# Kernel tuning notes

Hardware: AMD Instinct MI355X
Metric: run time of the kernel (lower is better)

The kernel has to match this reference:

```python
import jax, jax.numpy as jnp
import numpy as np

B, N, D = 2, 2048, 768
H = 12
HD = D // H  # 64

def setup_inputs() -> dict:
    key = jax.random.key(0)
    ks = jax.random.split(key, 5)
    scale = 1.0 / np.sqrt(D)
    return {
        "x": jax.random.normal(ks[0], (B, N, D), dtype=jnp.float32),
        "W_kqv": jax.random.normal(ks[1], (H, 3 * HD, D), dtype=jnp.float32) * scale,
        "b_kqv": jax.random.normal(ks[2], (H, 3 * HD), dtype=jnp.float32) * 0.01,
        "W_proj": jax.random.normal(ks[3], (D, D), dtype=jnp.float32) * scale,
        "b_proj": jax.random.normal(ks[4], (D,), dtype=jnp.float32) * 0.01,
    }

def reference(x, W_kqv, b_kqv, W_proj, b_proj):
    # Per-head Linear: x @ W_h^T + b_h, all heads at once -> [B, H, N, 3*HD]
    kqv = jnp.einsum('bnd,hod->bhno', x, W_kqv) + b_kqv[None, :, None, :]
    k, q, v = jnp.split(kqv, 3, axis=-1)  # each [B, H, N, HD]
    # scores = q @ k^T / sqrt(head_dim)  (attention_scores(a=k, b=q))
    scores = jnp.einsum('bhqd,bhkd->bhqk', q, k) / jnp.sqrt(jnp.asarray(HD, x.dtype))
    # causal mask (tril): masked_fill with -inf where mask == 0
    causal = jnp.tril(jnp.ones((N, N), dtype=bool))
    scores = jnp.where(causal[None, None, :, :], scores, -jnp.inf)
    attn = jax.nn.softmax(scores, axis=-1)
    sa = jnp.einsum('bhqk,bhkd->bhqd', attn, v)  # [B, H, N, HD]
    # concat heads along feature dim (head order preserved)
    sa = sa.transpose(0, 2, 1, 3).reshape(B, N, D)
    # output projection
    return sa @ W_proj.T + b_proj
```

## Files before the change

kernel.cpp:

```cpp
#include <hip/hip_runtime.h>

#define BB 2
#define SEQ 2048
#define DIM 768
#define NH 12
#define HD 64

typedef _Float16 half8 __attribute__((ext_vector_type(8)));
typedef _Float16 h4v __attribute__((ext_vector_type(4)));
typedef __fp16 f16x2 __attribute__((ext_vector_type(2)));
typedef float floatx4 __attribute__((ext_vector_type(4)));

__device__ __forceinline__ void gl_lds16(const _Float16* g, _Float16* l) {
    __builtin_amdgcn_global_load_lds(
        (const __attribute__((address_space(1))) void*)g,
        (__attribute__((address_space(3))) void*)l, 16, 0, 0);
}

__device__ __forceinline__ h4v pack4(float a, float b, float c, float d) {
    union { f16x2 h2[2]; h4v h4; } u;
    u.h2[0] = __builtin_amdgcn_cvt_pkrtz(a, b);
    u.h2[1] = __builtin_amdgcn_cvt_pkrtz(c, d);
    return u.h4;
}

__global__ __launch_bounds__(256)
void cvt3(const float* __restrict__ s0, _Float16* __restrict__ d0, int nb0,
          const float* __restrict__ s1, _Float16* __restrict__ d1, int nb1,
          const float* __restrict__ s2, _Float16* __restrict__ d2) {
    int b = blockIdx.x;
    const float* s; _Float16* d;
    if (b < nb0)            { s = s0; d = d0; }
    else if (b < nb0 + nb1) { s = s1; d = d1; b -= nb0; }
    else                    { s = s2; d = d2; b -= nb0 + nb1; }
    const int i = (b * 256 + threadIdx.x) * 8;
    float4 a = *(const float4*)(s + i);
    float4 c = *(const float4*)(s + i + 4);
    half8 h;
    h[0] = (_Float16)a.x; h[1] = (_Float16)a.y; h[2] = (_Float16)a.z; h[3] = (_Float16)a.w;
    h[4] = (_Float16)c.x; h[5] = (_Float16)c.y; h[6] = (_Float16)c.z; h[7] = (_Float16)c.w;
    *(half8*)(d + i) = h;
}

#define GEMM_CORE_P(APTR, BPTR)                                                 \
    __shared__ _Float16 Asl[3][128 * 32];                                       \
    __shared__ _Float16 Bsl[3][128 * 32];                                       \
    const int t = threadIdx.x, w = t >> 6, lane = t & 63;                       \
    const int quad = lane >> 4, l15 = lane & 15;                                \
    const int wm = w >> 1, wn = w & 1;                                          \
    const floatx4 z4 = {0.f, 0.f, 0.f, 0.f};                                    \
    floatx4 acc[4][4];                                                          \
    _Pragma("unroll") for (int i = 0; i < 4; ++i)                               \
        _Pragma("unroll") for (int j = 0; j < 4; ++j) acc[i][j] = z4;           \
    const _Float16* pA = APTR + (size_t)(m0 + w * 32 + l15) * DIM + quad * 8;   \
    const _Float16* pB = BPTR + (size_t)(c0 + w * 32 + l15) * DIM + quad * 8;   \
    _Pragma("unroll") for (int pt = 0; pt < 2; ++pt) {                          \
        gl_lds16(pA + pt * 32,            &Asl[pt][(w * 2 + 0) * 512]);         \
        gl_lds16(pA + pt * 32 + 16 * DIM, &Asl[pt][(w * 2 + 1) * 512]);         \
        gl_lds16(pB + pt * 32,            &Bsl[pt][(w * 2 + 0) * 512]);         \
        gl_lds16(pB + pt * 32 + 16 * DIM, &Bsl[pt][(w * 2 + 1) * 512]);         \
    }                                                                           \
    int cur = 0, pre = 2;                                                       \
    for (int it = 0; it < DIM / 32; ++it) {                                     \
        if (it + 1 < DIM / 32)                                                  \
            asm volatile("s_waitcnt vmcnt(4) lgkmcnt(0)" ::: "memory");         \
        else                                                                    \
            asm volatile("s_waitcnt vmcnt(0) lgkmcnt(0)" ::: "memory");         \
        __builtin_amdgcn_s_barrier();                                           \
        __builtin_amdgcn_sched_barrier(0);                                      \
        if (it + 2 < DIM / 32) {                                                \
            const int k2 = (it + 2) * 32;                                       \
            gl_lds16(pA + k2,            &Asl[pre][(w * 2 + 0) * 512]);         \
            gl_lds16(pA + k2 + 16 * DIM, &Asl[pre][(w * 2 + 1) * 512]);         \
            gl_lds16(pB + k2,            &Bsl[pre][(w * 2 + 0) * 512]);         \
            gl_lds16(pB + k2 + 16 * DIM, &Bsl[pre][(w * 2 + 1) * 512]);         \
        }                                                                       \
        half8 af[4], bf[4];                                                     \
        _Pragma("unroll") for (int i = 0; i < 4; ++i)                           \
            af[i] = *(const half8*)&Asl[cur][(wm * 4 + i) * 512 + lane * 8];    \
        _Pragma("unroll") for (int j = 0; j < 4; ++j)                           \
            bf[j] = *(const half8*)&Bsl[cur][(wn * 4 + j) * 512 + lane * 8];    \
        _Pragma("unroll") for (int i = 0; i < 4; ++i)                           \
            _Pragma("unroll") for (int j = 0; j < 4; ++j)                       \
                acc[i][j] = __builtin_amdgcn_mfma_f32_16x16x32_f16(             \
                    af[i], bf[j], acc[i][j], 0, 0, 0);                          \
        cur = (cur == 2) ? 0 : cur + 1;                                         \
        pre = (pre == 2) ? 0 : pre + 1;                                         \
    }

__global__ __launch_bounds__(256)
void kqv_gemm2(const _Float16* __restrict__ xh, const _Float16* __restrict__ Wh,
               const float* __restrict__ bias, _Float16* __restrict__ kb,
               _Float16* __restrict__ qb, _Float16* __restrict__ vbT) {
    const int hw = blockIdx.x;
    const int lg = (hw & 7) * 72 + (hw >> 3);
    const int m0 = (lg / 18) * 128, c0 = (lg % 18) * 128;
    GEMM_CORE_P(xh, Wh)
    #pragma unroll
    for (int j = 0; j < 4; ++j) {
        const int cbase = c0 + (wn * 4 + j) * 16;
        const int h = cbase / 192;
        const int rem = cbase - h * 192;
        const int part = rem >> 6;
        const float bv = bias[cbase + l15];
        const int d = (rem & 63) + l15;
        if (part == 2) {
            const int bidx = m0 >> 11;
            const int nb = (m0 & (SEQ - 1)) + wm * 64 + quad * 4;
            _Float16* vdst = vbT + ((size_t)(bidx * NH + h) * HD + d) * SEQ;
            #pragma unroll
            for (int i = 0; i < 4; ++i)
                *(h4v*)&vdst[nb + i * 16] =
                    pack4(acc[i][j][0] + bv, acc[i][j][1] + bv,
                          acc[i][j][2] + bv, acc[i][j][3] + bv);
        } else {
            _Float16* dst = (part == 0) ? kb : qb;
            #pragma unroll
            for (int i = 0; i < 4; ++i)
                #pragma unroll
                for (int r = 0; r < 4; ++r) {
                    const int m = m0 + (wm * 4 + i) * 16 + quad * 4 + r;
                    const int bidx = m >> 11, n = m & (SEQ - 1);
                    dst[(((size_t)(bidx * NH + h) * SEQ + n) << 6) + d] =
                        (_Float16)(acc[i][j][r] + bv);
                }
        }
    }
}

__global__ __launch_bounds__(256)
void proj_gemm2(const _Float16* __restrict__ A, const _Float16* __restrict__ Wh,
                const float* __restrict__ bias, float* __restrict__ out) {
    const int hw = blockIdx.x;
    const int lg = (hw & 7) * 24 + (hw >> 3);
    const int m0 = (lg / 6) * 128, c0 = (lg % 6) * 128;
    GEMM_CORE_P(A, Wh)
    #pragma unroll
    for (int j = 0; j < 4; ++j) {
        const int cbase = c0 + (wn * 4 + j) * 16;
        const float bv = bias[cbase + l15];
        #pragma unroll
        for (int i = 0; i < 4; ++i)
            #pragma unroll
            for (int r = 0; r < 4; ++r) {
                const int m = m0 + (wm * 4 + i) * 16 + quad * 4 + r;
                out[(size_t)m * DIM + cbase + l15] = acc[i][j][r] + bv;
            }
    }
}

__global__ __launch_bounds__(256)
void attn_mfma(const _Float16* __restrict__ qb, const _Float16* __restrict__ kbuf,
               const _Float16* __restrict__ vbT, _Float16* __restrict__ sa,
               _Float16* __restrict__ Opart, float* __restrict__ lpart) {
    __shared__ _Float16 Kl[2][64 * 64];
    __shared__ _Float16 Vl[2][64 * 64];
    __shared__ _Float16 Pl[4][16 * 64];
    const int hw = blockIdx.x;
    const int lg = (hw & 7) * 240 + (hw >> 3);
    const int bh = lg / 80;
    int u = lg % 80;
    int qt, p, np;
    if (u < 8)       { qt = u;                            p = 0;      np = 1; }
    else if (u < 24) { int v = u - 8;  qt = 8  + (v >> 1); p = v & 1; np = 2; }
    else if (u < 48) { int v = u - 24; qt = 16 + v / 3;    p = v % 3; np = 3; }
    else             { int v = u - 48; qt = 24 + (v >> 2); p = v & 3; np = 4; }
    const int kt0 = p * 8;
    const int ktn = (p == np - 1) ? (qt - kt0 + 1) : 8;

    const int t = threadIdx.x, w = t >> 6, lane = t & 63, quad = lane >> 4, l15 = lane & 15;
    const size_t base = (size_t)bh * (SEQ * HD);
    const int i0 = qt * 64 + w * 16;
    _Float16* Pw = Pl[w];
    const _Float16* Kg = kbuf + base;
    const _Float16* Vg = vbT + base;

    const int lr = lane >> 3, gg = lane & 7;
    const int gs = (gg ^ (lr & 7)) * 8;

    half8 aq[2];
    aq[0] = *(const half8*)(qb + base + (size_t)(i0 + l15) * HD + quad * 8);
    aq[1] = *(const half8*)(qb + base + (size_t)(i0 + l15) * HD + 32 + quad * 8);
    const _Float16 qs = (_Float16)(0.125f * 1.44269504f);
    #pragma unroll
    for (int k = 0; k < 8; ++k) { aq[0][k] *= qs; aq[1][k] *= qs; }

    const floatx4 z4 = {0.f, 0.f, 0.f, 0.f};
    floatx4 O[4];
    #pragma unroll
    for (int dt = 0; dt < 4; ++dt) O[dt] = z4;
    float l_one = 0.f;

    #pragma unroll
    for (int pp = 0; pp < 2; ++pp) {
        const int c = w * 2 + pp, row = c * 8 + lr;
        gl_lds16(Kg + (size_t)(kt0 * 64 + row) * HD + gs,  &Kl[0][c * 512]);
        gl_lds16(Vg + (size_t)row * SEQ + kt0 * 64 + gs,   &Vl[0][c * 512]);
    }

    const int swz = l15 & 7;
    const int sswz = (l15 & 7) << 1;
    const int srow = l15 * 64;

    for (int it = 0; it < ktn; ++it) {
        const int kt = kt0 + it;
        const int buf = it & 1;
        const int j0 = kt * 64;
        __syncthreads();

        if (it + 1 < ktn) {
            const _Float16* Kn = Kg + (size_t)(j0 + 64) * HD;
            const _Float16* Vn = Vg + (j0 + 64);
            #pragma unroll
            for (int pp = 0; pp < 2; ++pp) {
                const int c = w * 2 + pp, row = c * 8 + lr;
                gl_lds16(Kn + (size_t)row * HD + gs,  &Kl[buf ^ 1][c * 512]);
                gl_lds16(Vn + (size_t)row * SEQ + gs, &Vl[buf ^ 1][c * 512]);
            }
        }

        floatx4 S[4];
        #pragma unroll
        for (int nt = 0; nt < 4; ++nt) S[nt] = z4;
        __builtin_amdgcn_s_setprio(1);
        #pragma unroll
        for (int ks = 0; ks < 2; ++ks)
            #pragma unroll
            for (int nt = 0; nt < 4; ++nt) {
                half8 bk = *(const half8*)&Kl[buf][(nt * 16 + l15) * 64 +
                                                   (((ks * 4 + quad) ^ swz) << 3)];
                S[nt] = __builtin_amdgcn_mfma_f32_16x16x32_f16(bk, aq[ks], S[nt], 0, 0, 0);
            }
        __builtin_amdgcn_s_setprio(0);

        asm volatile("" ::: "memory");
        if (kt == qt) {
            #pragma unroll
            for (int nt = 0; nt < 4; ++nt) {
                float pv[4];
                #pragma unroll
                for (int r = 0; r < 4; ++r) {
                    float pvv = exp2f(S[nt][r]);
                    if (nt * 16 + quad * 4 + r > w * 16 + l15) pvv = 0.f;
                    l_one += pvv;
                    pv[r] = pvv;
                }
                *(h4v*)&Pw[srow + (((nt * 4 + quad) ^ sswz) << 2)] =
                    pack4(pv[0], pv[1], pv[2], pv[3]);
            }
        } else {
            #pragma unroll
            for (int nt = 0; nt < 4; ++nt) {
                float pv[4];
                #pragma unroll
                for (int r = 0; r < 4; ++r) {
                    float pvv = exp2f(S[nt][r]);
                    l_one += pvv;
                    pv[r] = pvv;
                }
                *(h4v*)&Pw[srow + (((nt * 4 + quad) ^ sswz) << 2)] =
                    pack4(pv[0], pv[1], pv[2], pv[3]);
            }
        }
        asm volatile("" ::: "memory");

        __builtin_amdgcn_s_setprio(1);
        #pragma unroll
        for (int ks = 0; ks < 2; ++ks) {
            half8 ap = *(const half8*)&Pw[srow + (((((ks * 4 + quad) << 1)) ^ sswz) << 2)];
            #pragma unroll
            for (int dt = 0; dt < 4; ++dt) {
                half8 bv = *(const half8*)&Vl[buf][(dt * 16 + l15) * 64 +
                                                    (((ks * 4 + quad) ^ swz) << 3)];
                O[dt] = __builtin_amdgcn_mfma_f32_16x16x32_f16(ap, bv, O[dt], 0, 0, 0);
            }
        }
        __builtin_amdgcn_s_setprio(0);
    }

    float rs = l_one;
    rs += __shfl_xor(rs, 16);
    rs += __shfl_xor(rs, 32);

    if (np == 1) {
        const float inv = 1.0f / rs;
        const int bidx = bh / NH, h = bh - bidx * NH;
        #pragma unroll
        for (int r = 0; r < 4; ++r) {
            const float invr = __shfl(inv, quad * 4 + r);
            const int i = i0 + quad * 4 + r;
            #pragma unroll
            for (int dt = 0; dt < 4; ++dt)
                sa[(size_t)(bidx * SEQ + i) * DIM + h * HD + dt * 16 + l15] =
                    (_Float16)(O[dt][r] * invr);
        }
    } else {
        const size_t slot = ((size_t)(bh * 32 + qt) * 4 + p);
        _Float16* Od = Opart + slot * 4096;
        float*    ld = lpart + slot * 64;
        if (lane < 16) ld[w * 16 + lane] = rs;
        #pragma unroll
        for (int r = 0; r < 4; ++r) {
            const int row = w * 16 + quad * 4 + r;
            #pragma unroll
            for (int dt = 0; dt < 4; ++dt)
                Od[row * 64 + dt * 16 + l15] = (_Float16)O[dt][r];
        }
    }
}

__global__ __launch_bounds__(256)
void attn_combine(const _Float16* __restrict__ Opart, const float* __restrict__ lpart,
                  _Float16* __restrict__ sa) {
    const int qt = 8 + blockIdx.x;
    const int bh = blockIdx.y;
    const int np = (qt >> 3) + 1;
    const int t = threadIdx.x;
    const int row = t >> 2, d0 = (t & 3) * 16;
    const size_t slot0 = ((size_t)(bh * 32 + qt) * 4);

    float lsum = 0.f;
    for (int p = 0; p < np; ++p) lsum += lpart[(slot0 + p) * 64 + row];

    float acc[16];
    #pragma unroll
    for (int k = 0; k < 16; ++k) acc[k] = 0.f;
    for (int p = 0; p < np; ++p) {
        const _Float16* src = Opart + (slot0 + p) * 4096 + row * 64 + d0;
        half8 a = *(const half8*)src;
        half8 b = *(const half8*)(src + 8);
        #pragma unroll
        for (int k = 0; k < 8; ++k) { acc[k] += (float)a[k]; acc[8 + k] += (float)b[k]; }
    }
    const float inv = 1.0f / lsum;
    const int bidx = bh / NH, h = bh - bidx * NH;
    _Float16* dst = sa + (size_t)(bidx * SEQ + qt * 64 + row) * DIM + h * HD + d0;
    half8 o0, o1;
    #pragma unroll
    for (int k = 0; k < 8; ++k) { o0[k] = (_Float16)(acc[k] * inv); o1[k] = (_Float16)(acc[8 + k] * inv); }
    *(half8*)dst       = o0;
    *(half8*)(dst + 8) = o1;
}

extern "C" void kernel_launch(void* const* d_in, const int* in_sizes, int n_in,
                              void* d_out, int out_size, void* d_ws, size_t ws_size,
                              hipStream_t stream) {
    (void)in_sizes; (void)n_in; (void)out_size; (void)ws_size;
    const float* x  = (const float*)d_in[0];
    const float* Wk = (const float*)d_in[1];
    const float* bk = (const float*)d_in[2];
    const float* Wp = (const float*)d_in[3];
    const float* bp = (const float*)d_in[4];
    float* out = (float*)d_out;

    _Float16* ws = (_Float16*)d_ws;
    const size_t per = (size_t)BB * NH * SEQ * HD;
    const int nx = BB * SEQ * DIM;
    const int nwk = NH * 3 * HD * DIM;
    const int nwp = DIM * DIM;
    _Float16* kb  = ws;
    _Float16* qb  = ws + per;
    _Float16* vbT = ws + 3 * per;
    _Float16* sa  = ws + 4 * per;
    _Float16* xh  = ws + 5 * per;
    _Float16* Wkh = xh + nx;
    _Float16* Wph = Wkh + nwk;
    _Float16* Opart = Wph + nwp;
    float*    lpart = (float*)(Opart + (size_t)24 * 32 * 4 * 4096);

    const int nb0 = nx / 2048, nb1 = nwk / 2048, nb2 = nwp / 2048;
    cvt3<<<dim3(nb0 + nb1 + nb2), 256, 0, stream>>>(x, xh, nb0, Wk, Wkh, nb1, Wp, Wph);

    kqv_gemm2  <<<dim3(576), 256, 0, stream>>>(xh, Wkh, bk, kb, qb, vbT);
    attn_mfma  <<<dim3(1920), 256, 0, stream>>>(qb, kb, vbT, sa, Opart, lpart);
    attn_combine<<<dim3(24, 24), 256, 0, stream>>>(Opart, lpart, sa);
    proj_gemm2 <<<dim3(192), 256, 0, stream>>>(sa, Wph, bp, out);
}
```

Measured before the change: 174.5 us.

## Double attention query tile to 128 rows per block for K/V reuse

Each attention block now handles 128 query rows (32 per wave, two 16-row groups) instead of 64, so every K/V tile loaded into LDS serves twice as many queries. The grid halves to 960 blocks, the key-split mapping is recomputed for 16 query tiles, and the partial-output combine kernel is resized to 128-row slots. Per-wave work skips fully masked key tiles and applies the mask only on diagonal tiles. In exchange there are fewer blocks for load balancing and higher register and LDS use.

```diff
diff --git a/kernel.cpp b/kernel.cpp
--- a/kernel.cpp
+++ b/kernel.cpp
@@ -155,22 +155,23 @@
                _Float16* __restrict__ Opart, float* __restrict__ lpart) {
     __shared__ _Float16 Kl[2][64 * 64];
     __shared__ _Float16 Vl[2][64 * 64];
-    __shared__ _Float16 Pl[4][16 * 64];
+    __shared__ _Float16 Pl[4][32 * 64];
     const int hw = blockIdx.x;
-    const int lg = (hw & 7) * 240 + (hw >> 3);
-    const int bh = lg / 80;
-    int u = lg % 80;
-    int qt, p, np;
-    if (u < 8)       { qt = u;                            p = 0;      np = 1; }
-    else if (u < 24) { int v = u - 8;  qt = 8  + (v >> 1); p = v & 1; np = 2; }
-    else if (u < 48) { int v = u - 24; qt = 16 + v / 3;    p = v % 3; np = 3; }
-    else             { int v = u - 48; qt = 24 + (v >> 2); p = v & 3; np = 4; }
+    const int lg = (hw & 7) * 120 + (hw >> 3);
+    const int bh = lg / 40;
+    int u = lg % 40;
+    int qt2, p, np;
+    if (u < 4)       { qt2 = u;                              p = 0;      np = 1; }
+    else if (u < 12) { int v = u - 4;  qt2 = 4  + (v >> 1);  p = v & 1;  np = 2; }
+    else if (u < 24) { int v = u - 12; qt2 = 8  + v / 3;     p = v % 3;  np = 3; }
+    else             { int v = u - 24; qt2 = 12 + (v >> 2);  p = v & 3;  np = 4; }
+    const int T = 2 * qt2 + 2;
     const int kt0 = p * 8;
-    const int ktn = (p == np - 1) ? (qt - kt0 + 1) : 8;
+    const int ktn = (p == np - 1) ? (T - kt0) : 8;
 
     const int t = threadIdx.x, w = t >> 6, lane = t & 63, quad = lane >> 4, l15 = lane & 15;
     const size_t base = (size_t)bh * (SEQ * HD);
-    const int i0 = qt * 64 + w * 16;
+    const int i0 = qt2 * 128 + w * 32;
     _Float16* Pw = Pl[w];
     const _Float16* Kg = kbuf + base;
     const _Float16* Vg = vbT + base;
@@ -178,18 +179,26 @@
     const int lr = lane >> 3, gg = lane & 7;
     const int gs = (gg ^ (lr & 7)) * 8;
 
-    half8 aq[2];
-    aq[0] = *(const half8*)(qb + base + (size_t)(i0 + l15) * HD + quad * 8);
-    aq[1] = *(const half8*)(qb + base + (size_t)(i0 + l15) * HD + 32 + quad * 8);
+    half8 aq[2][2];
+    #pragma unroll
+    for (int rg = 0; rg < 2; ++rg) {
+        const _Float16* qrow = qb + base + (size_t)(i0 + rg * 16 + l15) * HD;
+        aq[rg][0] = *(const half8*)(qrow + quad * 8);
+        aq[rg][1] = *(const half8*)(qrow + 32 + quad * 8);
+    }
     const _Float16 qs = (_Float16)(0.125f * 1.44269504f);
     #pragma unroll
-    for (int k = 0; k < 8; ++k) { aq[0][k] *= qs; aq[1][k] *= qs; }
+    for (int rg = 0; rg < 2; ++rg)
+        #pragma unroll
+        for (int k = 0; k < 8; ++k) { aq[rg][0][k] *= qs; aq[rg][1][k] *= qs; }
 
     const floatx4 z4 = {0.f, 0.f, 0.f, 0.f};
-    floatx4 O[4];
-    #pragma unroll
-    for (int dt = 0; dt < 4; ++dt) O[dt] = z4;
-    float l_one = 0.f;
+    floatx4 O[2][4];
+    #pragma unroll
+    for (int rg = 0; rg < 2; ++rg)
+        #pragma unroll
+        for (int dt = 0; dt < 4; ++dt) O[rg][dt] = z4;
+    float l_one[2] = {0.f, 0.f};
 
     #pragma unroll
     for (int pp = 0; pp < 2; ++pp) {
@@ -200,7 +209,6 @@
 
     const int swz = l15 & 7;
     const int sswz = (l15 & 7) << 1;
-    const int srow = l15 * 64;
 
     for (int it = 0; it < ktn; ++it) {
         const int kt = kt0 + it;
@@ -219,92 +227,112 @@
             }
         }
 
-        floatx4 S[4];
-        #pragma unroll
-        for (int nt = 0; nt < 4; ++nt) S[nt] = z4;
-        __builtin_amdgcn_s_setprio(1);
-        #pragma unroll
-        for (int ks = 0; ks < 2; ++ks)
-            #pragma unroll
-            for (int nt = 0; nt < 4; ++nt) {
-                half8 bk = *(const half8*)&Kl[buf][(nt * 16 + l15) * 64 +
-                                                   (((ks * 4 + quad) ^ swz) << 3)];
-                S[nt] = __builtin_amdgcn_mfma_f32_16x16x32_f16(bk, aq[ks], S[nt], 0, 0, 0);
+        const bool active = (j0 <= i0 + 31);
+        const bool diag   = (j0 + 63 > i0);
+        if (active) {
+            #pragma unroll
+            for (int rg = 0; rg < 2; ++rg) {
+                const int srow = (rg * 16 + l15) * 64;
+                floatx4 S[4];
+                #pragma unroll
+                for (int nt = 0; nt < 4; ++nt) S[nt] = z4;
+                __builtin_amdgcn_s_setprio(1);
+                #pragma unroll
+                for (int ks = 0; ks < 2; ++ks)
+                    #pragma unroll
+                    for (int nt = 0; nt < 4; ++nt) {
+                        half8 bk = *(const half8*)&Kl[buf][(nt * 16 + l15) * 64 +
+                                                           (((ks * 4 + quad) ^ swz) << 3)];
+                        S[nt] = __builtin_amdgcn_mfma_f32_16x16x32_f16(bk, aq[rg][ks], S[nt], 0, 0, 0);
+                    }
+                __builtin_amdgcn_s_setprio(0);
+
+                asm volatile("" ::: "memory");
+                if (diag) {
+                    const int iq = i0 + rg * 16 + l15;
+                    #pragma unroll
+                    for (int nt = 0; nt < 4; ++nt) {
+                        float pv[4];
+                        #pragma unroll
+                        for (int r = 0; r < 4; ++r) {
+                            float pvv = exp2f(S[nt][r]);
+                            if (j0 + nt * 16 + quad * 4 + r > iq) pvv = 0.f;
+                            l_one[rg] += pvv;
+                            pv[r] = pvv;
+                        }
+                        *(h4v*)&Pw[srow + (((nt * 4 + quad) ^ sswz) << 2)] =
+                            pack4(pv[0], pv[1], pv[2], pv[3]);
+                    }
+                } else {
+                    #pragma unroll
+                    for (int nt = 0; nt < 4; ++nt) {
+                        float pv[4];
+                        #pragma unroll
+                        for (int r = 0; r < 4; ++r) {
+                            float pvv = exp2f(S[nt][r]);
+                            l_one[rg] += pvv;
+                            pv[r] = pvv;
+                        }
+                        *(h4v*)&Pw[srow + (((nt * 4 + quad) ^ sswz) << 2)] =
+                            pack4(pv[0], pv[1], pv[2], pv[3]);
+                    }
+                }
+                asm volatile("" ::: "memory");
+
+                __builtin_amdgcn_s_setprio(1);
+                #pragma unroll
+                for (int ks = 0; ks < 2; ++ks) {
+                    half8 ap = *(const half8*)&Pw[srow + (((((ks * 4 + quad) << 1)) ^ sswz) << 2)];
+                    #pragma unroll
+                    for (int dt = 0; dt < 4; ++dt) {
+                        half8 bv = *(const half8*)&Vl[buf][(dt * 16 + l15) * 64 +
+                                                            (((ks * 4 + quad) ^ swz) << 3)];
+                        O[rg][dt] = __builtin_amdgcn_mfma_f32_16x16x32_f16(ap, bv, O[rg][dt], 0, 0, 0);
+                    }
+                }
+                __builtin_amdgcn_s_setprio(0);
             }
-        __builtin_amdgcn_s_setprio(0);
-
-        asm volatile("" ::: "memory");
-        if (kt == qt) {
-            #pragma unroll
-            for (int nt = 0; nt < 4; ++nt) {
-                float pv[4];
-                #pragma unroll
-                for (int r = 0; r < 4; ++r) {
-                    float pvv = exp2f(S[nt][r]);
-                    if (nt * 16 + quad * 4 + r > w * 16 + l15) pvv = 0.f;
-                    l_one += pvv;
-                    pv[r] = pvv;
-                }
-                *(h4v*)&Pw[srow + (((nt * 4 + quad) ^ sswz) << 2)] =
-                    pack4(pv[0], pv[1], pv[2], pv[3]);
+        }
+    }
+
+    float rs[2];
+    #pragma unroll
+    for (int rg = 0; rg < 2; ++rg) {
+        float v = l_one[rg];
+        v += __shfl_xor(v, 16);
+        v += __shfl_xor(v, 32);
+        rs[rg] = v;
+    }
+
+    if (np == 1) {
+        const int bidx = bh / NH, h = bh - bidx * NH;
+        #pragma unroll
+        for (int rg = 0; rg < 2; ++rg) {
+            const float inv = 1.0f / rs[rg];
+            #pragma unroll
+            for (int r = 0; r < 4; ++r) {
+                const float invr = __shfl(inv, quad * 4 + r);
+                const int i = i0 + rg * 16 + quad * 4 + r;
+                #pragma unroll
+                for (int dt = 0; dt < 4; ++dt)
+                    sa[(size_t)(bidx * SEQ + i) * DIM + h * HD + dt * 16 + l15] =
+                        (_Float16)(O[rg][dt][r] * invr);
             }
-        } else {
-            #pragma unroll
-            for (int nt = 0; nt < 4; ++nt) {
-                float pv[4];
-                #pragma unroll
-                for (int r = 0; r < 4; ++r) {
-                    float pvv = exp2f(S[nt][r]);
-                    l_one += pvv;
-                    pv[r] = pvv;
-                }
-                *(h4v*)&Pw[srow + (((nt * 4 + quad) ^ sswz) << 2)] =
-                    pack4(pv[0], pv[1], pv[2], pv[3]);
+        }
+    } else {
+        const size_t slot = ((size_t)(bh * 16 + qt2) * 4 + p);
+        _Float16* Od = Opart + slot * 8192;
+        float*    ld = lpart + slot * 128;
+        #pragma unroll
+        for (int rg = 0; rg < 2; ++rg) {
+            if (lane < 16) ld[w * 32 + rg * 16 + lane] = rs[rg];
+            #pragma unroll
+            for (int r = 0; r < 4; ++r) {
+                const int row = w * 32 + rg * 16 + quad * 4 + r;
+                #pragma unroll
+                for (int dt = 0; dt < 4; ++dt)
+                    Od[row * 64 + dt * 16 + l15] = (_Float16)O[rg][dt][r];
             }
-        }
-        asm volatile("" ::: "memory");
-
-        __builtin_amdgcn_s_setprio(1);
-        #pragma unroll
-        for (int ks = 0; ks < 2; ++ks) {
-            half8 ap = *(const half8*)&Pw[srow + (((((ks * 4 + quad) << 1)) ^ sswz) << 2)];
-            #pragma unroll
-            for (int dt = 0; dt < 4; ++dt) {
-                half8 bv = *(const half8*)&Vl[buf][(dt * 16 + l15) * 64 +
-                                                    (((ks * 4 + quad) ^ swz) << 3)];
-                O[dt] = __builtin_amdgcn_mfma_f32_16x16x32_f16(ap, bv, O[dt], 0, 0, 0);
-            }
-        }
-        __builtin_amdgcn_s_setprio(0);
-    }
-
-    float rs = l_one;
-    rs += __shfl_xor(rs, 16);
-    rs += __shfl_xor(rs, 32);
-
-    if (np == 1) {
-        const float inv = 1.0f / rs;
-        const int bidx = bh / NH, h = bh - bidx * NH;
-        #pragma unroll
-        for (int r = 0; r < 4; ++r) {
-            const float invr = __shfl(inv, quad * 4 + r);
-            const int i = i0 + quad * 4 + r;
-            #pragma unroll
-            for (int dt = 0; dt < 4; ++dt)
-                sa[(size_t)(bidx * SEQ + i) * DIM + h * HD + dt * 16 + l15] =
-                    (_Float16)(O[dt][r] * invr);
-        }
-    } else {
-        const size_t slot = ((size_t)(bh * 32 + qt) * 4 + p);
-        _Float16* Od = Opart + slot * 4096;
-        float*    ld = lpart + slot * 64;
-        if (lane < 16) ld[w * 16 + lane] = rs;
-        #pragma unroll
-        for (int r = 0; r < 4; ++r) {
-            const int row = w * 16 + quad * 4 + r;
-            #pragma unroll
-            for (int dt = 0; dt < 4; ++dt)
-                Od[row * 64 + dt * 16 + l15] = (_Float16)O[dt][r];
         }
     }
 }
@@ -312,34 +340,38 @@
 __global__ __launch_bounds__(256)
 void attn_combine(const _Float16* __restrict__ Opart, const float* __restrict__ lpart,
                   _Float16* __restrict__ sa) {
-    const int qt = 8 + blockIdx.x;
+    const int qt2 = 4 + blockIdx.x;
     const int bh = blockIdx.y;
-    const int np = (qt >> 3) + 1;
+    const int np = (2 * qt2 + 2 + 7) >> 3;
     const int t = threadIdx.x;
-    const int row = t >> 2, d0 = (t & 3) * 16;
-    const size_t slot0 = ((size_t)(bh * 32 + qt) * 4);
+    const int row = t >> 1, d0 = (t & 1) * 32;
+    const size_t slot0 = ((size_t)(bh * 16 + qt2) * 4);
 
     float lsum = 0.f;
-    for (int p = 0; p < np; ++p) lsum += lpart[(slot0 + p) * 64 + row];
-
-    float acc[16];
-    #pragma unroll
-    for (int k = 0; k < 16; ++k) acc[k] = 0.f;
+    for (int p = 0; p < np; ++p) lsum += lpart[(slot0 + p) * 128 + row];
+
+    float acc[32];
+    #pragma unroll
+    for (int k = 0; k < 32; ++k) acc[k] = 0.f;
     for (int p = 0; p < np; ++p) {
-        const _Float16* src = Opart + (slot0 + p) * 4096 + row * 64 + d0;
-        half8 a = *(const half8*)src;
-        half8 b = *(const half8*)(src + 8);
-        #pragma unroll
-        for (int k = 0; k < 8; ++k) { acc[k] += (float)a[k]; acc[8 + k] += (float)b[k]; }
+        const _Float16* src = Opart + (slot0 + p) * 8192 + row * 64 + d0;
+        #pragma unroll
+        for (int v = 0; v < 4; ++v) {
+            half8 a = *(const half8*)(src + v * 8);
+            #pragma unroll
+            for (int k = 0; k < 8; ++k) acc[v * 8 + k] += (float)a[k];
+        }
     }
     const float inv = 1.0f / lsum;
     const int bidx = bh / NH, h = bh - bidx * NH;
-    _Float16* dst = sa + (size_t)(bidx * SEQ + qt * 64 + row) * DIM + h * HD + d0;
-    half8 o0, o1;
-    #pragma unroll
-    for (int k = 0; k < 8; ++k) { o0[k] = (_Float16)(acc[k] * inv); o1[k] = (_Float16)(acc[8 + k] * inv); }
-    *(half8*)dst       = o0;
-    *(half8*)(dst + 8) = o1;
+    _Float16* dst = sa + (size_t)(bidx * SEQ + qt2 * 128 + row) * DIM + h * HD + d0;
+    #pragma unroll
+    for (int v = 0; v < 4; ++v) {
+        half8 o;
+        #pragma unroll
+        for (int k = 0; k < 8; ++k) o[k] = (_Float16)(acc[v * 8 + k] * inv);
+        *(half8*)(dst + v * 8) = o;
+    }
 }
 
 extern "C" void kernel_launch(void* const* d_in, const int* in_sizes, int n_in,
@@ -366,13 +398,13 @@
     _Float16* Wkh = xh + nx;
     _Float16* Wph = Wkh + nwk;
     _Float16* Opart = Wph + nwp;
-    float*    lpart = (float*)(Opart + (size_t)24 * 32 * 4 * 4096);
+    float*    lpart = (float*)(Opart + (size_t)24 * 16 * 4 * 8192);
 
     const int nb0 = nx / 2048, nb1 = nwk / 2048, nb2 = nwp / 2048;
     cvt3<<<dim3(nb0 + nb1 + nb2), 256, 0, stream>>>(x, xh, nb0, Wk, Wkh, nb1, Wp, Wph);
 
     kqv_gemm2  <<<dim3(576), 256, 0, stream>>>(xh, Wkh, bk, kb, qb, vbT);
-    attn_mfma  <<<dim3(1920), 256, 0, stream>>>(qb, kb, vbT, sa, Opart, lpart);
-    attn_combine<<<dim3(24, 24), 256, 0, stream>>>(Opart, lpart, sa);
+    attn_mfma  <<<dim3(960), 256, 0, stream>>>(qb, kb, vbT, sa, Opart, lpart);
+    attn_combine<<<dim3(12, 24), 256, 0, stream>>>(Opart, lpart, sa);
     proj_gemm2 <<<dim3(192), 256, 0, stream>>>(sa, Wph, bp, out);
 }
```

Result: slower. 182.9 us (+4.8%).

## Double attention query tile to 128 rows with 512-thread blocks sharing K/V tiles

Applied to the files above, without the earlier changes.

Each attention block now handles 128 query rows with 8 waves instead of 64 rows with 4 waves. The K/V tiles staged in LDS are therefore shared by twice as many waves, which halves global K/V traffic per query row and lets each wave issue a single load per tile. The split-K partitioning, partial-output slots and the combine kernel are rescaled to match. Waves whose rows lie entirely above the current key tile now skip it, and the causal mask uses absolute indices. The trade-offs are coarser causal load balancing, idle waves on diagonal tiles, and larger blocks that may reduce occupancy.

```diff
diff --git a/kernel.cpp b/kernel.cpp
--- a/kernel.cpp
+++ b/kernel.cpp
@@ -149,28 +149,29 @@
     }
 }
 
-__global__ __launch_bounds__(256)
+__global__ __launch_bounds__(512, 6)
 void attn_mfma(const _Float16* __restrict__ qb, const _Float16* __restrict__ kbuf,
                const _Float16* __restrict__ vbT, _Float16* __restrict__ sa,
                _Float16* __restrict__ Opart, float* __restrict__ lpart) {
     __shared__ _Float16 Kl[2][64 * 64];
     __shared__ _Float16 Vl[2][64 * 64];
-    __shared__ _Float16 Pl[4][16 * 64];
+    __shared__ _Float16 Pl[8][16 * 64];
     const int hw = blockIdx.x;
-    const int lg = (hw & 7) * 240 + (hw >> 3);
-    const int bh = lg / 80;
-    int u = lg % 80;
-    int qt, p, np;
-    if (u < 8)       { qt = u;                            p = 0;      np = 1; }
-    else if (u < 24) { int v = u - 8;  qt = 8  + (v >> 1); p = v & 1; np = 2; }
-    else if (u < 48) { int v = u - 24; qt = 16 + v / 3;    p = v % 3; np = 3; }
-    else             { int v = u - 48; qt = 24 + (v >> 2); p = v & 3; np = 4; }
+    const int lg = (hw & 7) * 120 + (hw >> 3);
+    const int bh = lg / 40;
+    int u = lg % 40;
+    int qt2, p, np;
+    if (u < 4)       { qt2 = u;                              p = 0;      np = 1; }
+    else if (u < 12) { int v = u - 4;  qt2 = 4  + (v >> 1);  p = v & 1;  np = 2; }
+    else if (u < 24) { int v = u - 12; qt2 = 8  + v / 3;     p = v % 3;  np = 3; }
+    else             { int v = u - 24; qt2 = 12 + (v >> 2);  p = v & 3;  np = 4; }
+    const int T = 2 * qt2 + 2;
     const int kt0 = p * 8;
-    const int ktn = (p == np - 1) ? (qt - kt0 + 1) : 8;
+    const int ktn = (p == np - 1) ? (T - kt0) : 8;
 
     const int t = threadIdx.x, w = t >> 6, lane = t & 63, quad = lane >> 4, l15 = lane & 15;
     const size_t base = (size_t)bh * (SEQ * HD);
-    const int i0 = qt * 64 + w * 16;
+    const int i0 = qt2 * 128 + w * 16;
     _Float16* Pw = Pl[w];
     const _Float16* Kg = kbuf + base;
     const _Float16* Vg = vbT + base;
@@ -191,11 +192,10 @@
     for (int dt = 0; dt < 4; ++dt) O[dt] = z4;
     float l_one = 0.f;
 
-    #pragma unroll
-    for (int pp = 0; pp < 2; ++pp) {
-        const int c = w * 2 + pp, row = c * 8 + lr;
-        gl_lds16(Kg + (size_t)(kt0 * 64 + row) * HD + gs,  &Kl[0][c * 512]);
-        gl_lds16(Vg + (size_t)row * SEQ + kt0 * 64 + gs,   &Vl[0][c * 512]);
+    {
+        const int row = w * 8 + lr;
+        gl_lds16(Kg + (size_t)(kt0 * 64 + row) * HD + gs,  &Kl[0][w * 512]);
+        gl_lds16(Vg + (size_t)row * SEQ + kt0 * 64 + gs,   &Vl[0][w * 512]);
     }
 
     const int swz = l15 & 7;
@@ -211,13 +211,14 @@
         if (it + 1 < ktn) {
             const _Float16* Kn = Kg + (size_t)(j0 + 64) * HD;
             const _Float16* Vn = Vg + (j0 + 64);
-            #pragma unroll
-            for (int pp = 0; pp < 2; ++pp) {
-                const int c = w * 2 + pp, row = c * 8 + lr;
-                gl_lds16(Kn + (size_t)row * HD + gs,  &Kl[buf ^ 1][c * 512]);
-                gl_lds16(Vn + (size_t)row * SEQ + gs, &Vl[buf ^ 1][c * 512]);
-            }
-        }
+            const int row = w * 8 + lr;
+            gl_lds16(Kn + (size_t)row * HD + gs,  &Kl[buf ^ 1][w * 512]);
+            gl_lds16(Vn + (size_t)row * SEQ + gs, &Vl[buf ^ 1][w * 512]);
+        }
+
+        const bool active = (j0 <= i0 + 15);
+        if (!active) continue;
+        const bool diag = (j0 + 63 > i0);
 
         floatx4 S[4];
         #pragma unroll
@@ -234,14 +235,15 @@
         __builtin_amdgcn_s_setprio(0);
 
         asm volatile("" ::: "memory");
-        if (kt == qt) {
+        if (diag) {
+            const int iq = i0 + l15;
             #pragma unroll
             for (int nt = 0; nt < 4; ++nt) {
                 float pv[4];
                 #pragma unroll
                 for (int r = 0; r < 4; ++r) {
                     float pvv = exp2f(S[nt][r]);
-                    if (nt * 16 + quad * 4 + r > w * 16 + l15) pvv = 0.f;
+                    if (j0 + nt * 16 + quad * 4 + r > iq) pvv = 0.f;
                     l_one += pvv;
                     pv[r] = pvv;
                 }
@@ -295,9 +297,9 @@
                     (_Float16)(O[dt][r] * invr);
         }
     } else {
-        const size_t slot = ((size_t)(bh * 32 + qt) * 4 + p);
-        _Float16* Od = Opart + slot * 4096;
-        float*    ld = lpart + slot * 64;
+        const size_t slot = ((size_t)(bh * 16 + qt2) * 4 + p);
+        _Float16* Od = Opart + slot * 8192;
+        float*    ld = lpart + slot * 128;
         if (lane < 16) ld[w * 16 + lane] = rs;
         #pragma unroll
         for (int r = 0; r < 4; ++r) {
@@ -312,34 +314,38 @@
 __global__ __launch_bounds__(256)
 void attn_combine(const _Float16* __restrict__ Opart, const float* __restrict__ lpart,
                   _Float16* __restrict__ sa) {
-    const int qt = 8 + blockIdx.x;
+    const int qt2 = 4 + blockIdx.x;
     const int bh = blockIdx.y;
-    const int np = (qt >> 3) + 1;
+    const int np = (2 * qt2 + 2 + 7) >> 3;
     const int t = threadIdx.x;
-    const int row = t >> 2, d0 = (t & 3) * 16;
-    const size_t slot0 = ((size_t)(bh * 32 + qt) * 4);
+    const int row = t >> 1, d0 = (t & 1) * 32;
+    const size_t slot0 = ((size_t)(bh * 16 + qt2) * 4);
 
     float lsum = 0.f;
-    for (int p = 0; p < np; ++p) lsum += lpart[(slot0 + p) * 64 + row];
-
-    float acc[16];
-    #pragma unroll
-    for (int k = 0; k < 16; ++k) acc[k] = 0.f;
+    for (int p = 0; p < np; ++p) lsum += lpart[(slot0 + p) * 128 + row];
+
+    float acc[32];
+    #pragma unroll
+    for (int k = 0; k < 32; ++k) acc[k] = 0.f;
     for (int p = 0; p < np; ++p) {
-        const _Float16* src = Opart + (slot0 + p) * 4096 + row * 64 + d0;
-        half8 a = *(const half8*)src;
-        half8 b = *(const half8*)(src + 8);
-        #pragma unroll
-        for (int k = 0; k < 8; ++k) { acc[k] += (float)a[k]; acc[8 + k] += (float)b[k]; }
+        const _Float16* src = Opart + (slot0 + p) * 8192 + row * 64 + d0;
+        #pragma unroll
+        for (int v = 0; v < 4; ++v) {
+            half8 a = *(const half8*)(src + v * 8);
+            #pragma unroll
+            for (int k = 0; k < 8; ++k) acc[v * 8 + k] += (float)a[k];
+        }
     }
     const float inv = 1.0f / lsum;
     const int bidx = bh / NH, h = bh - bidx * NH;
-    _Float16* dst = sa + (size_t)(bidx * SEQ + qt * 64 + row) * DIM + h * HD + d0;
-    half8 o0, o1;
-    #pragma unroll
-    for (int k = 0; k < 8; ++k) { o0[k] = (_Float16)(acc[k] * inv); o1[k] = (_Float16)(acc[8 + k] * inv); }
-    *(half8*)dst       = o0;
-    *(half8*)(dst + 8) = o1;
+    _Float16* dst = sa + (size_t)(bidx * SEQ + qt2 * 128 + row) * DIM + h * HD + d0;
+    #pragma unroll
+    for (int v = 0; v < 4; ++v) {
+        half8 o;
+        #pragma unroll
+        for (int k = 0; k < 8; ++k) o[k] = (_Float16)(acc[v * 8 + k] * inv);
+        *(half8*)(dst + v * 8) = o;
+    }
 }
 
 extern "C" void kernel_launch(void* const* d_in, const int* in_sizes, int n_in,
@@ -366,13 +372,13 @@
     _Float16* Wkh = xh + nx;
     _Float16* Wph = Wkh + nwk;
     _Float16* Opart = Wph + nwp;
-    float*    lpart = (float*)(Opart + (size_t)24 * 32 * 4 * 4096);
+    float*    lpart = (float*)(Opart + (size_t)24 * 16 * 4 * 8192);
 
     const int nb0 = nx / 2048, nb1 = nwk / 2048, nb2 = nwp / 2048;
     cvt3<<<dim3(nb0 + nb1 + nb2), 256, 0, stream>>>(x, xh, nb0, Wk, Wkh, nb1, Wp, Wph);
 
     kqv_gemm2  <<<dim3(576), 256, 0, stream>>>(xh, Wkh, bk, kb, qb, vbT);
-    attn_mfma  <<<dim3(1920), 256, 0, stream>>>(qb, kb, vbT, sa, Opart, lpart);
-    attn_combine<<<dim3(24, 24), 256, 0, stream>>>(Opart, lpart, sa);
+    attn_mfma  <<<dim3(960), 512, 0, stream>>>(qb, kb, vbT, sa, Opart, lpart);
+    attn_combine<<<dim3(12, 24), 256, 0, stream>>>(Opart, lpart, sa);
     proj_gemm2 <<<dim3(192), 256, 0, stream>>>(sa, Wph, bp, out);
 }
```

New measurement: 175.4 us. About the same (+0.5%).
